# Kernel optimization log

Hardware: AMD Instinct MI355X
Metric: run time of the kernel (lower is better)

## Reference

```python
import jax, jax.numpy as jnp
import numpy as np

NEG_SLOPE = 0.1

def lrelu(x):
    return jnp.where(x >= 0, x, NEG_SLOPE * x)

def conv2d(x, w, b, padding=0, dilation=1):
    y = jax.lax.conv_general_dilated(
        x, w, window_strides=(1, 1),
        padding=[(padding, padding), (padding, padding)],
        rhs_dilation=(dilation, dilation),
        dimension_numbers=('NCHW', 'OIHW', 'NCHW'))
    return y + b[None, :, None, None]

def res_aspp(x, p):
    r1 = lrelu(conv2d(x, p['a1_w'], p['a1_b'], padding=1, dilation=1))
    r2 = lrelu(conv2d(x, p['a2_w'], p['a2_b'], padding=2, dilation=2))
    r3 = lrelu(conv2d(x, p['a3_w'], p['a3_b'], padding=4, dilation=4))
    r = conv2d(jnp.concatenate((r1, r2, r3), axis=1), p['ar_w'], p['ar_b'])
    return x + r

def deform_conv2d(x, offset, w, b):
    # x: [B,C,H,W], offset: [B,2*K,H,W] torchvision layout (y,x) per 3x3 tap
    B, C, H, W = x.shape
    KH = KW = 3
    K = KH * KW
    pad = 1
    off = offset.reshape(B, K, 2, H, W)
    ky, kx = jnp.meshgrid(jnp.arange(KH), jnp.arange(KW), indexing='ij')
    ky = ky.reshape(K).astype(x.dtype)
    kx = kx.reshape(K).astype(x.dtype)
    hh = jnp.arange(H, dtype=x.dtype)
    ww = jnp.arange(W, dtype=x.dtype)
    # sampling positions [B,K,H,W]
    py = off[:, :, 0] + (hh[None, None, :, None] - pad + ky[None, :, None, None])
    px = off[:, :, 1] + (ww[None, None, None, :] - pad + kx[None, :, None, None])
    y0 = jnp.floor(py)
    x0 = jnp.floor(px)
    wy = (py - y0)[:, None]  # [B,1,K,H,W]
    wx = (px - x0)[:, None]
    y0i = y0.astype(jnp.int32)
    x0i = x0.astype(jnp.int32)
    x_flat = x.reshape(B, C, H * W)

    def gather(iy, ix):
        valid = ((iy >= 0) & (iy < H) & (ix >= 0) & (ix < W)).astype(x.dtype)
        idx = jnp.clip(iy, 0, H - 1) * W + jnp.clip(ix, 0, W - 1)  # [B,K,H,W]
        v = jax.vmap(lambda xb, ib: xb[:, ib])(x_flat, idx.reshape(B, -1))
        return v.reshape(B, C, K, H, W) * valid[:, None]

    samp = (gather(y0i, x0i) * (1 - wy) * (1 - wx)
            + gather(y0i, x0i + 1) * (1 - wy) * wx
            + gather(y0i + 1, x0i) * wy * (1 - wx)
            + gather(y0i + 1, x0i + 1) * wy * wx)
    out = jnp.einsum('bckhw,ock->bohw', samp, w.reshape(w.shape[0], C, K))
    return out + b[None, :, None, None]

def setup_inputs() -> dict:
    key = jax.random.key(0)
    ks = jax.random.split(key, 16)
    B, C, H, W = 4, 64, 160, 160
    Cout = 64
    s = 0.05
    d = {
        'in_aux': jax.random.normal(ks[0], (B, C, H, W), jnp.float32),
        'in_ref': jax.random.normal(ks[1], (B, C, H, W), jnp.float32),
        'w01': jax.random.normal(ks[2], (Cout, 2 * C, 1, 1), jnp.float32) * s,
        'b01': jnp.zeros((Cout,), jnp.float32),
        'a1_w': jax.random.normal(ks[3], (Cout, Cout, 3, 3), jnp.float32) * s,
        'a1_b': jnp.zeros((Cout,), jnp.float32),
        'a2_w': jax.random.normal(ks[4], (Cout, Cout, 3, 3), jnp.float32) * s,
        'a2_b': jnp.zeros((Cout,), jnp.float32),
        'a3_w': jax.random.normal(ks[5], (Cout, Cout, 3, 3), jnp.float32) * s,
        'a3_b': jnp.zeros((Cout,), jnp.float32),
        'ar_w': jax.random.normal(ks[6], (Cout, 3 * Cout, 1, 1), jnp.float32) * s,
        'ar_b': jnp.zeros((Cout,), jnp.float32),
        'w02': jax.random.normal(ks[7], (18, Cout, 1, 1), jnp.float32) * s,
        'b02': jnp.zeros((18,), jnp.float32),
        'dw': jax.random.normal(ks[8], (Cout, C, 3, 3), jnp.float32) * s,
        'db': jnp.zeros((Cout,), jnp.float32),
    }
    return d

def reference(in_aux, in_ref, w01, b01, a1_w, a1_b, a2_w, a2_b, a3_w, a3_b,
              ar_w, ar_b, w02, b02, dw, db):
    cat_x = jnp.concatenate((in_aux, in_ref), axis=1)
    off_x = lrelu(conv2d(cat_x, w01, b01))
    p = {'a1_w': a1_w, 'a1_b': a1_b, 'a2_w': a2_w, 'a2_b': a2_b,
         'a3_w': a3_w, 'a3_b': a3_b, 'ar_w': ar_w, 'ar_b': ar_b}
    off_x = res_aspp(off_x, p)
    off_x = conv2d(off_x, w02, b02)
    return deform_conv2d(in_aux, off_x, dw, db)
```

## Files before the change

### kernel.cpp

```cpp
#include <hip/hip_runtime.h>
#include <math.h>

static constexpr int B = 4, H = 160, W = 160;
static constexpr int HW = H * W;
static constexpr int CHW = 64 * HW;
static constexpr int NELEM = B * CHW;

typedef short bf16x8 __attribute__((ext_vector_type(8)));
typedef float f32x4 __attribute__((ext_vector_type(4)));

__device__ __forceinline__ float lrelu(float v) { return v >= 0.f ? v : 0.1f * v; }

__device__ __forceinline__ unsigned short f2bf(float f) {
  unsigned u = __float_as_uint(f);
  return (unsigned short)((u + 0x7FFFu + ((u >> 16) & 1u)) >> 16);
}
__device__ __forceinline__ float bf2f(short u) {
  return __uint_as_float(((unsigned)(unsigned short)u) << 16);
}

__global__ __launch_bounds__(256) void k_transform(
    const float* __restrict__ w01, const float* __restrict__ dw,
    const float* __restrict__ arw, const float* __restrict__ a1w,
    const float* __restrict__ a2w, const float* __restrict__ a3w,
    unsigned short* __restrict__ w01_bf, unsigned short* __restrict__ wb_bf,
    unsigned short* __restrict__ wd_bf, unsigned short* __restrict__ arw_bf) {
  int i = blockIdx.x * 256 + threadIdx.x;
  if (i < 8192) {
    w01_bf[i] = f2bf(w01[i]);
  } else if (i < 118784) {
    int j = i - 8192;
    int ci = j & 63, co = (j >> 6) & 63;
    int kk = j >> 12;
    int dsel = kk / 9; kk -= dsel * 9;
    const float* src = dsel == 0 ? a1w : dsel == 1 ? a2w : a3w;
    wb_bf[j] = f2bf(src[(co * 64 + ci) * 9 + kk]);
  } else if (i < 155648) {
    int j = i - 118784;
    int ci = j & 63, co = (j >> 6) & 63, k = j >> 12;
    wd_bf[j] = f2bf(dw[(co * 64 + ci) * 9 + k]);
  } else if (i < 167936) {
    int j = i - 155648;
    arw_bf[j] = f2bf(arw[j]);
  }
}

__global__ __launch_bounds__(256) void k_conv1x1_mfma(
    const float* __restrict__ aux, const float* __restrict__ ref,
    const unsigned short* __restrict__ w01_bf, const float* __restrict__ b01,
    float* __restrict__ off0p, unsigned short* __restrict__ off0_bf,
    unsigned short* __restrict__ x_bf) {
  __shared__ unsigned short sa[64 * 144];
  int pos0 = blockIdx.x * 64;
  int b = pos0 / HW;
  int hw0 = pos0 - b * HW;
  int tid = threadIdx.x;
#pragma unroll 4
  for (int it = 0; it < 32; ++it) {
    int i = it * 256 + tid;
    int ci = i >> 6, p = i & 63;
    float v = (ci < 64) ? aux[b * CHW + ci * HW + hw0 + p]
                        : ref[b * CHW + (ci - 64) * HW + hw0 + p];
    int key = (p >> 2) & 7;
    sa[p * 144 + (((ci >> 3) ^ key) * 8) + (ci & 7)] = f2bf(v);
  }
  __syncthreads();
  int lane = tid & 63, wid = tid >> 6;
  int m = lane & 15, q = lane >> 4;
  f32x4 acc[4] = {};
#pragma unroll
  for (int kc = 0; kc < 4; ++kc) {
    bf16x8 bfrag = *(const bf16x8*)(w01_bf + (wid * 16 + m) * 128 + kc * 32 + q * 8);
#pragma unroll
    for (int mt = 0; mt < 4; ++mt) {
      int row = mt * 16 + m;
      int rkey = (row >> 2) & 7;
      bf16x8 afrag = *(const bf16x8*)(sa + row * 144 + (((kc * 4 + q) ^ rkey) * 8));
      acc[mt] = __builtin_amdgcn_mfma_f32_16x16x32_bf16(afrag, bfrag, acc[mt],
                                                        0, 0, 0);
    }
  }
#pragma unroll
  for (int it = 0; it < 2; ++it) {
    int u = it * 256 + tid;
    int p = u >> 3, c = u & 7;
    int key = (p >> 2) & 7;
    uint4 v = *(const uint4*)(sa + p * 144 + ((c ^ key) * 8));
    *(uint4*)(x_bf + ((size_t)(b * HW + hw0 + p)) * 64 + c * 8) = v;
  }
  float bi = b01[wid * 16 + m];
  float vv[4][4];
#pragma unroll
  for (int mt = 0; mt < 4; ++mt)
#pragma unroll
    for (int r = 0; r < 4; ++r) {
      float v = lrelu(acc[mt][r] + bi);
      vv[mt][r] = v;
      off0p[((size_t)(b * HW + hw0 + mt * 16 + q * 4 + r)) * 64 + wid * 16 + m] = v;
    }
  __syncthreads();
#pragma unroll
  for (int mt = 0; mt < 4; ++mt)
#pragma unroll
    for (int r = 0; r < 4; ++r) {
      int pl = mt * 16 + q * 4 + r;
      int chunk = wid * 2 + (m >> 3);
      int key = (pl >> 2) & 7;
      sa[pl * 80 + ((chunk ^ key) * 8) + (m & 7)] = f2bf(vv[mt][r]);
    }
  __syncthreads();
#pragma unroll
  for (int it = 0; it < 2; ++it) {
    int u = it * 256 + tid;
    int p = u >> 3, c = u & 7;
    int key = (p >> 2) & 7;
    uint4 v = *(const uint4*)(sa + p * 80 + ((c ^ key) * 8));
    *(uint4*)(off0_bf + ((size_t)(b * HW + hw0 + p)) * 64 + c * 8) = v;
  }
}

__global__ __launch_bounds__(256) void k_aspp3_mfma(
    const unsigned short* __restrict__ off0_bf,
    const unsigned short* __restrict__ wb_bf,
    const float* __restrict__ a1b, const float* __restrict__ a2b,
    const float* __restrict__ a3b, unsigned short* __restrict__ r_bf) {
  __shared__ unsigned short epb[256 * 80];
  int bx = blockIdx.x, by = blockIdx.y;
  int dsel = blockIdx.z >> 2, b = blockIdx.z & 3;
  int d = 1 << dsel;
  const float* bias = dsel == 0 ? a1b : dsel == 1 ? a2b : a3b;
  int tid = threadIdx.x;
  int lane = tid & 63, wid = tid >> 6;
  int m = lane & 15, q = lane >> 4;
  f32x4 acc[4][4] = {};
  const unsigned short* wbase = wb_bf + dsel * 9 * 4096;
  const unsigned short* xoff = off0_bf + (size_t)b * HW * 64;
  int ybase = by * 16 + wid * 4;
  int xcol = bx * 16 + m;

#pragma unroll 3
  for (int k = 0; k < 9; ++k) {
    int ky = k / 3, kx = k - ky * 3;
    int gx = xcol + (kx - 1) * d;
    bool vx = (unsigned)gx < (unsigned)W;
    int gy[4];
    bool vy[4];
#pragma unroll
    for (int mt = 0; mt < 4; ++mt) {
      gy[mt] = ybase + mt + (ky - 1) * d;
      vy[mt] = (unsigned)gy[mt] < (unsigned)H;
    }
#pragma unroll
    for (int ch = 0; ch < 2; ++ch) {
      bf16x8 bfrag[4];
#pragma unroll
      for (int t = 0; t < 4; ++t)
        bfrag[t] =
            *(const bf16x8*)(wbase + (k * 64 + t * 16 + m) * 64 + ch * 32 + q * 8);
      bf16x8 afrag[4];
#pragma unroll
      for (int mt = 0; mt < 4; ++mt) {
        bf16x8 z = {0, 0, 0, 0, 0, 0, 0, 0};
        afrag[mt] = z;
        if (vy[mt] && vx)
          afrag[mt] = *(const bf16x8*)(xoff + ((size_t)(gy[mt] * W + gx)) * 64 +
                                       ch * 32 + q * 8);
      }
#pragma unroll
      for (int mt = 0; mt < 4; ++mt)
#pragma unroll
        for (int t = 0; t < 4; ++t)
          acc[mt][t] = __builtin_amdgcn_mfma_f32_16x16x32_bf16(
              afrag[mt], bfrag[t], acc[mt][t], 0, 0, 0);
    }
  }

#pragma unroll
  for (int t = 0; t < 4; ++t) {
    float bi = bias[t * 16 + m];
#pragma unroll
    for (int mt = 0; mt < 4; ++mt) {
      int prow = wid * 4 + mt;
#pragma unroll
      for (int r = 0; r < 4; ++r) {
        int pix = prow * 16 + q * 4 + r;
        int chunk = t * 2 + (m >> 3);
        int key = (pix >> 2) & 7;
        epb[pix * 80 + ((chunk ^ key) * 8) + (m & 7)] =
            f2bf(lrelu(acc[mt][t][r] + bi));
      }
    }
  }
  __syncthreads();
  {
    int pix = tid;
    int prow = pix >> 4, pcol = pix & 15;
    int key = (pix >> 2) & 7;
    unsigned short* dst =
        r_bf + ((size_t)(b * HW + (by * 16 + prow) * W + bx * 16 + pcol)) * 192 +
        dsel * 64;
#pragma unroll
    for (int c = 0; c < 8; ++c)
      *(uint4*)(dst + c * 8) = *(const uint4*)(epb + pix * 80 + ((c ^ key) * 8));
  }
}

__global__ __launch_bounds__(256) void k_merge_head_mfma(
    const unsigned short* __restrict__ r_bf, const float* __restrict__ off0p,
    const unsigned short* __restrict__ arw_bf, const float* __restrict__ arb,
    const float* __restrict__ w02, const float* __restrict__ b02,
    float* __restrict__ offs) {
  __shared__ unsigned short sa[64 * 200];
  int pos0 = blockIdx.x * 64;
  int b = pos0 / HW;
  int hw0 = pos0 - b * HW;
  int tid = threadIdx.x;
  const unsigned short* gsrc = r_bf + (size_t)(b * HW + hw0) * 192;
  for (int i = tid; i < 1536; i += 256) {
    int pos = i / 24, c8 = i - pos * 24;
    *(uint4*)(sa + pos * 200 + c8 * 8) = *(const uint4*)(gsrc + i * 8);
  }
  __syncthreads();
  int lane = tid & 63, wid = tid >> 6;
  int m = lane & 15, q = lane >> 4;
  f32x4 acc[4] = {};
#pragma unroll
  for (int kc = 0; kc < 6; ++kc) {
    bf16x8 bfrag = *(const bf16x8*)(arw_bf + (wid * 16 + m) * 192 + kc * 32 + q * 8);
#pragma unroll
    for (int mt = 0; mt < 4; ++mt) {
      bf16x8 afrag = *(const bf16x8*)(sa + (mt * 16 + m) * 200 + kc * 32 + q * 8);
      acc[mt] = __builtin_amdgcn_mfma_f32_16x16x32_bf16(afrag, bfrag, acc[mt],
                                                        0, 0, 0);
    }
  }
  __syncthreads();
  float* ep = (float*)sa;
  int co = wid * 16 + m;
  float bi = arb[co];
  const float* resb = off0p + (size_t)(b * HW + hw0) * 64;
#pragma unroll
  for (int mt = 0; mt < 4; ++mt)
#pragma unroll
    for (int r = 0; r < 4; ++r) {
      int pos = mt * 16 + q * 4 + r;
      ep[pos * 65 + co] = acc[mt][r] + bi + resb[pos * 64 + co];
    }
  __syncthreads();
  for (int i = tid; i < 1152; i += 256) {
    int t = i >> 6, p = i & 63;
    const float* w2 = w02 + t * 64;
    float o = b02[t];
#pragma unroll 8
    for (int c = 0; c < 64; ++c) o += ep[p * 65 + c] * w2[c];
    offs[(b * 18 + t) * HW + hw0 + p] = o;
  }
}

__global__ __launch_bounds__(256) void k_deform_mfma(
    const unsigned short* __restrict__ x_bf, const float* __restrict__ offs,
    const unsigned short* __restrict__ wd_bf, const float* __restrict__ db,
    float* __restrict__ out) {
  constexpr int SP = 72;
  __shared__ unsigned short sb[2][64 * SP];
  int blk = (blockIdx.x & 7) * 200 + (blockIdx.x >> 3);
  int pos0 = blk * 64;
  int b = pos0 / HW;
  int hw0 = pos0 - b * HW;
  int tid = threadIdx.x;
  int lane = tid & 63, wid = tid >> 6;
  int m = lane & 15, q = lane >> 4;
  int p = lane;
  int cg = wid;
  int hw = hw0 + p;
  int h = hw / W, wv = hw - h * W;
  const unsigned short* xb = x_bf + (size_t)b * HW * 64;
  const float* ob = offs + b * 18 * HW + hw;
  float offv[18];
#pragma unroll
  for (int j = 0; j < 18; ++j) offv[j] = ob[j * HW];
  f32x4 acc[4] = {};

#pragma unroll
  for (int k = 0; k < 9; ++k) {
    const int ky = k / 3, kx = k - ky * 3;
    float py = offv[2 * k] + (float)(h - 1 + ky);
    float px = offv[2 * k + 1] + (float)(wv - 1 + kx);
    float fy = floorf(py), fx = floorf(px);
    int iy0 = (int)fy, ix0 = (int)fx;
    float wy = py - fy, wx = px - fx;
    int iy1 = iy0 + 1, ix1 = ix0 + 1;
    float vy0 = (iy0 >= 0 && iy0 < H) ? 1.f : 0.f;
    float vy1 = (iy1 >= 0 && iy1 < H) ? 1.f : 0.f;
    float vx0 = (ix0 >= 0 && ix0 < W) ? 1.f : 0.f;
    float vx1 = (ix1 >= 0 && ix1 < W) ? 1.f : 0.f;
    int cy0 = min(max(iy0, 0), H - 1), cy1 = min(max(iy1, 0), H - 1);
    int cx0 = min(max(ix0, 0), W - 1), cx1 = min(max(ix1, 0), W - 1);
    float c00 = vy0 * vx0 * (1.f - wy) * (1.f - wx);
    float c01 = vy0 * vx1 * (1.f - wy) * wx;
    float c10 = vy1 * vx0 * wy * (1.f - wx);
    float c11 = vy1 * vx1 * wy * wx;
    const unsigned short* p00 = xb + (size_t)(cy0 * W + cx0) * 64 + cg * 16;
    const unsigned short* p01 = xb + (size_t)(cy0 * W + cx1) * 64 + cg * 16;
    const unsigned short* p10 = xb + (size_t)(cy1 * W + cx0) * 64 + cg * 16;
    const unsigned short* p11 = xb + (size_t)(cy1 * W + cx1) * 64 + cg * 16;
    unsigned short tb[16];
#pragma unroll
    for (int c2 = 0; c2 < 2; ++c2) {
      bf16x8 v00 = *(const bf16x8*)(p00 + c2 * 8);
      bf16x8 v01 = *(const bf16x8*)(p01 + c2 * 8);
      bf16x8 v10 = *(const bf16x8*)(p10 + c2 * 8);
      bf16x8 v11 = *(const bf16x8*)(p11 + c2 * 8);
#pragma unroll
      for (int j = 0; j < 8; ++j) {
        float sv = c00 * bf2f(v00[j]) + c01 * bf2f(v01[j]) +
                   c10 * bf2f(v10[j]) + c11 * bf2f(v11[j]);
        tb[c2 * 8 + j] = f2bf(sv);
      }
    }
    unsigned short* wr = &sb[k & 1][p * SP + cg * 16];
    *(uint4*)wr = *(const uint4*)&tb[0];
    *(uint4*)(wr + 8) = *(const uint4*)&tb[8];
    __syncthreads();
    const unsigned short* rb = &sb[k & 1][0];
#pragma unroll
    for (int kc = 0; kc < 2; ++kc) {
      bf16x8 bfrag =
          *(const bf16x8*)(wd_bf + (k * 64 + wid * 16 + m) * 64 + kc * 32 + q * 8);
#pragma unroll
      for (int mt = 0; mt < 4; ++mt) {
        bf16x8 afrag = *(const bf16x8*)(rb + (mt * 16 + m) * SP + kc * 32 + q * 8);
        acc[mt] = __builtin_amdgcn_mfma_f32_16x16x32_bf16(afrag, bfrag, acc[mt],
                                                          0, 0, 0);
      }
    }
  }
  int co = wid * 16 + m;
  float bias = db[co];
  size_t orow = (size_t)(b * 64 + co) * HW + hw0;
#pragma unroll
  for (int mt = 0; mt < 4; ++mt)
#pragma unroll
    for (int r = 0; r < 4; ++r)
      out[orow + mt * 16 + q * 4 + r] = acc[mt][r] + bias;
}

extern "C" void kernel_launch(void* const* d_in, const int* in_sizes, int n_in,
                              void* d_out, int out_size, void* d_ws, size_t ws_size,
                              hipStream_t stream) {
  const float* aux = (const float*)d_in[0];
  const float* ref = (const float*)d_in[1];
  const float* w01 = (const float*)d_in[2];
  const float* b01 = (const float*)d_in[3];
  const float* a1w = (const float*)d_in[4];
  const float* a1b = (const float*)d_in[5];
  const float* a2w = (const float*)d_in[6];
  const float* a2b = (const float*)d_in[7];
  const float* a3w = (const float*)d_in[8];
  const float* a3b = (const float*)d_in[9];
  const float* arw = (const float*)d_in[10];
  const float* arb = (const float*)d_in[11];
  const float* w02 = (const float*)d_in[12];
  const float* b02 = (const float*)d_in[13];
  const float* dw  = (const float*)d_in[14];
  const float* db  = (const float*)d_in[15];
  float* out = (float*)d_out;

  float* off0p = (float*)d_ws;
  float* offs = off0p + NELEM;
  unsigned short* w01_bf = (unsigned short*)(offs + B * 18 * HW);
  unsigned short* off0_bf = w01_bf + 8192;
  unsigned short* x_bf   = off0_bf + (size_t)NELEM;
  unsigned short* wb_bf  = x_bf + (size_t)NELEM;
  unsigned short* wd_bf  = wb_bf + 110592;
  unsigned short* arw_bf = wd_bf + 36864;
  unsigned short* r_bf   = arw_bf + 12288;

  k_transform<<<656, 256, 0, stream>>>(w01, dw, arw, a1w, a2w, a3w,
                                       w01_bf, wb_bf, wd_bf, arw_bf);
  k_conv1x1_mfma<<<B * HW / 64, 256, 0, stream>>>(aux, ref, w01_bf, b01,
                                                  off0p, off0_bf, x_bf);
  k_aspp3_mfma<<<dim3(10, 10, 12), 256, 0, stream>>>(
      off0_bf, wb_bf, a1b, a2b, a3b, r_bf);
  k_merge_head_mfma<<<B * HW / 64, 256, 0, stream>>>(
      r_bf, off0p, arw_bf, arb, w02, b02, offs);
  k_deform_mfma<<<B * HW / 64, 256, 0, stream>>>(x_bf, offs, wd_bf, db, out);
}
```

Before: 333.4 us.

## Store ASPP input in zero-padded halo layout and shrink epilogue LDS

```diff
diff --git a/kernel.cpp b/kernel.cpp
--- a/kernel.cpp
+++ b/kernel.cpp
@@ -5,6 +5,8 @@
 static constexpr int HW = H * W;
 static constexpr int CHW = 64 * HW;
 static constexpr int NELEM = B * CHW;
+static constexpr int PH = 168, PW = 168;
+static constexpr int PHW = PH * PW;
 
 typedef short bf16x8 __attribute__((ext_vector_type(8)));
 typedef float f32x4 __attribute__((ext_vector_type(4)));
@@ -48,7 +50,7 @@
 __global__ __launch_bounds__(256) void k_conv1x1_mfma(
     const float* __restrict__ aux, const float* __restrict__ ref,
     const unsigned short* __restrict__ w01_bf, const float* __restrict__ b01,
-    float* __restrict__ off0p, unsigned short* __restrict__ off0_bf,
+    float* __restrict__ off0p, unsigned short* __restrict__ off0_pad,
     unsigned short* __restrict__ x_bf) {
   __shared__ unsigned short sa[64 * 144];
   int pos0 = blockIdx.x * 64;
@@ -115,16 +117,19 @@
     int p = u >> 3, c = u & 7;
     int key = (p >> 2) & 7;
     uint4 v = *(const uint4*)(sa + p * 80 + ((c ^ key) * 8));
-    *(uint4*)(off0_bf + ((size_t)(b * HW + hw0 + p)) * 64 + c * 8) = v;
-  }
-}
-
-__global__ __launch_bounds__(256) void k_aspp3_mfma(
-    const unsigned short* __restrict__ off0_bf,
+    int hw = hw0 + p;
+    int h = hw / W, w = hw - h * W;
+    *(uint4*)(off0_pad +
+              ((size_t)(b * PHW + (h + 4) * PW + w + 4)) * 64 + c * 8) = v;
+  }
+}
+
+__global__ __launch_bounds__(256, 4) void k_aspp3_mfma(
+    const unsigned short* __restrict__ off0_pad,
     const unsigned short* __restrict__ wb_bf,
     const float* __restrict__ a1b, const float* __restrict__ a2b,
     const float* __restrict__ a3b, unsigned short* __restrict__ r_bf) {
-  __shared__ unsigned short epb[256 * 80];
+  __shared__ float ep[64 * 65];
   int bx = blockIdx.x, by = blockIdx.y;
   int dsel = blockIdx.z >> 2, b = blockIdx.z & 3;
   int d = 1 << dsel;
@@ -134,22 +139,15 @@
   int m = lane & 15, q = lane >> 4;
   f32x4 acc[4][4] = {};
   const unsigned short* wbase = wb_bf + dsel * 9 * 4096;
-  const unsigned short* xoff = off0_bf + (size_t)b * HW * 64;
-  int ybase = by * 16 + wid * 4;
-  int xcol = bx * 16 + m;
-
-#pragma unroll 3
+  const unsigned short* xb = off0_pad + (size_t)b * PHW * 64;
+  int ybase = by * 16 + wid * 4 + 4;
+  int xcol = bx * 16 + m + 4;
+
+#pragma unroll
   for (int k = 0; k < 9; ++k) {
     int ky = k / 3, kx = k - ky * 3;
     int gx = xcol + (kx - 1) * d;
-    bool vx = (unsigned)gx < (unsigned)W;
-    int gy[4];
-    bool vy[4];
-#pragma unroll
-    for (int mt = 0; mt < 4; ++mt) {
-      gy[mt] = ybase + mt + (ky - 1) * d;
-      vy[mt] = (unsigned)gy[mt] < (unsigned)H;
-    }
+    int gy0 = ybase + (ky - 1) * d;
 #pragma unroll
     for (int ch = 0; ch < 2; ++ch) {
       bf16x8 bfrag[4];
@@ -159,13 +157,9 @@
             *(const bf16x8*)(wbase + (k * 64 + t * 16 + m) * 64 + ch * 32 + q * 8);
       bf16x8 afrag[4];
 #pragma unroll
-      for (int mt = 0; mt < 4; ++mt) {
-        bf16x8 z = {0, 0, 0, 0, 0, 0, 0, 0};
-        afrag[mt] = z;
-        if (vy[mt] && vx)
-          afrag[mt] = *(const bf16x8*)(xoff + ((size_t)(gy[mt] * W + gx)) * 64 +
-                                       ch * 32 + q * 8);
-      }
+      for (int mt = 0; mt < 4; ++mt)
+        afrag[mt] = *(const bf16x8*)(xb + ((size_t)((gy0 + mt) * PW + gx)) * 64 +
+                                     ch * 32 + q * 8);
 #pragma unroll
       for (int mt = 0; mt < 4; ++mt)
 #pragma unroll
@@ -175,33 +169,35 @@
     }
   }
 
-#pragma unroll
-  for (int t = 0; t < 4; ++t) {
-    float bi = bias[t * 16 + m];
-#pragma unroll
-    for (int mt = 0; mt < 4; ++mt) {
-      int prow = wid * 4 + mt;
-#pragma unroll
-      for (int r = 0; r < 4; ++r) {
-        int pix = prow * 16 + q * 4 + r;
-        int chunk = t * 2 + (m >> 3);
-        int key = (pix >> 2) & 7;
-        epb[pix * 80 + ((chunk ^ key) * 8) + (m & 7)] =
-            f2bf(lrelu(acc[mt][t][r] + bi));
-      }
-    }
-  }
-  __syncthreads();
-  {
-    int pix = tid;
-    int prow = pix >> 4, pcol = pix & 15;
-    int key = (pix >> 2) & 7;
-    unsigned short* dst =
-        r_bf + ((size_t)(b * HW + (by * 16 + prow) * W + bx * 16 + pcol)) * 192 +
-        dsel * 64;
-#pragma unroll
-    for (int c = 0; c < 8; ++c)
-      *(uint4*)(dst + c * 8) = *(const uint4*)(epb + pix * 80 + ((c ^ key) * 8));
+  float bi[4];
+#pragma unroll
+  for (int t = 0; t < 4; ++t) bi[t] = bias[t * 16 + m];
+  for (int pass = 0; pass < 4; ++pass) {
+    if (pass) __syncthreads();
+    if (wid == pass) {
+#pragma unroll
+      for (int mt = 0; mt < 4; ++mt)
+#pragma unroll
+        for (int t = 0; t < 4; ++t)
+#pragma unroll
+          for (int r = 0; r < 4; ++r)
+            ep[(mt * 16 + q * 4 + r) * 65 + t * 16 + m] = acc[mt][t][r] + bi[t];
+    }
+    __syncthreads();
+#pragma unroll
+    for (int it = 0; it < 2; ++it) {
+      int u = it * 256 + tid;
+      int l = u >> 3, c = u & 7;
+      const float* src = ep + l * 65 + c * 8;
+      unsigned short tb[8];
+#pragma unroll
+      for (int j = 0; j < 8; ++j) tb[j] = f2bf(lrelu(src[j]));
+      int gl = pass * 64 + l;
+      int prow = gl >> 4, pcol = gl & 15;
+      *(uint4*)(r_bf +
+                ((size_t)(b * HW + (by * 16 + prow) * W + bx * 16 + pcol)) * 192 +
+                dsel * 64 + c * 8) = *(const uint4*)&tb[0];
+    }
   }
 }
 
@@ -369,19 +365,21 @@
   float* off0p = (float*)d_ws;
   float* offs = off0p + NELEM;
   unsigned short* w01_bf = (unsigned short*)(offs + B * 18 * HW);
-  unsigned short* off0_bf = w01_bf + 8192;
-  unsigned short* x_bf   = off0_bf + (size_t)NELEM;
+  unsigned short* off0_pad = w01_bf + 8192;
+  unsigned short* x_bf   = off0_pad + (size_t)B * PHW * 64;
   unsigned short* wb_bf  = x_bf + (size_t)NELEM;
   unsigned short* wd_bf  = wb_bf + 110592;
   unsigned short* arw_bf = wd_bf + 36864;
   unsigned short* r_bf   = arw_bf + 12288;
 
+  hipMemsetAsync(off0_pad, 0, (size_t)B * PHW * 64 * sizeof(unsigned short),
+                 stream);
   k_transform<<<656, 256, 0, stream>>>(w01, dw, arw, a1w, a2w, a3w,
                                        w01_bf, wb_bf, wd_bf, arw_bf);
   k_conv1x1_mfma<<<B * HW / 64, 256, 0, stream>>>(aux, ref, w01_bf, b01,
-                                                  off0p, off0_bf, x_bf);
+                                                  off0p, off0_pad, x_bf);
   k_aspp3_mfma<<<dim3(10, 10, 12), 256, 0, stream>>>(
-      off0_bf, wb_bf, a1b, a2b, a3b, r_bf);
+      off0_pad, wb_bf, a1b, a2b, a3b, r_bf);
   k_merge_head_mfma<<<B * HW / 64, 256, 0, stream>>>(
       r_bf, off0p, arw_bf, arb, w02, b02, offs);
   k_deform_mfma<<<B * HW / 64, 256, 0, stream>>>(x_bf, offs, wd_bf, db, out);
```

Result: no change. 338.4 us (+1.5%).
